# Optimization experiments

Hardware: AMD Instinct MI355X
Metric: run time of the kernel (lower is better)

Reference implementation:

```python
import jax, jax.numpy as jnp
import numpy as np

B, R, C, NC = 8, 1000, 1024, 81
H, W = 1024, 1024
MEANS = jnp.array([0.0, 0.0, 0.0, 0.0], jnp.float32)
STDS = jnp.array([0.1, 0.1, 0.2, 0.2], jnp.float32)
MIN_CONF = 0.05
NMS_THR = 0.5
MAX_INST = 100
NEG = -1e9


def setup_inputs() -> dict:
    key = jax.random.key(0)
    k1, k2, k3, k4, k5 = jax.random.split(key, 5)
    x = jax.random.normal(k1, (B * R, C), jnp.float32)
    w_cls = jax.random.normal(k2, (C, NC), jnp.float32) * 0.01
    b_cls = jnp.zeros((NC,), jnp.float32)
    w_delta = jax.random.normal(k3, (C, 4), jnp.float32) * 0.01
    b_delta = jnp.zeros((4,), jnp.float32)
    # rois: (batch_ind, y1, x1, y2, x2), normalized coords with y1<y2, x1<x2
    yx1 = jax.random.uniform(k4, (B * R, 2), jnp.float32) * 0.7
    hw = jax.random.uniform(k5, (B * R, 2), jnp.float32) * 0.28 + 0.02
    bind = jnp.repeat(jnp.arange(B, dtype=jnp.float32), R)[:, None]
    rois = jnp.concatenate([bind, yx1, yx1 + hw], axis=1)
    return {"x": x, "w_cls": w_cls, "b_cls": b_cls, "w_delta": w_delta, "b_delta": b_delta, "rois": rois}


def delta2bbox(rois, deltas):
    # rois, deltas: [N, 4] in (y1, x1, y2, x2) / (dy, dx, dh, dw)
    d = deltas * STDS + MEANS
    h = rois[:, 2] - rois[:, 0]
    w = rois[:, 3] - rois[:, 1]
    cy = rois[:, 0] + 0.5 * h + d[:, 0] * h
    cx = rois[:, 1] + 0.5 * w + d[:, 1] * w
    h = h * jnp.exp(d[:, 2])
    w = w * jnp.exp(d[:, 3])
    return jnp.stack([cy - 0.5 * h, cx - 0.5 * w, cy + 0.5 * h, cx + 0.5 * w], axis=1)


def pairwise_iou(boxes):
    # boxes: [N, 4]
    area = (boxes[:, 2] - boxes[:, 0]) * (boxes[:, 3] - boxes[:, 1])
    y1 = jnp.maximum(boxes[:, None, 0], boxes[None, :, 0])
    x1 = jnp.maximum(boxes[:, None, 1], boxes[None, :, 1])
    y2 = jnp.minimum(boxes[:, None, 2], boxes[None, :, 2])
    x2 = jnp.minimum(boxes[:, None, 3], boxes[None, :, 3])
    inter = jnp.maximum(y2 - y1, 0.0) * jnp.maximum(x2 - x1, 0.0)
    union = area[:, None] + area[None, :] - inter
    return inter / jnp.maximum(union, 1e-8)


def nms_single(boxes, scores, class_ids, valid):
    # boxes [R,4], scores [R], class_ids [R] int, valid [R] bool -> detections [MAX_INST, 6]
    masked = jnp.where(valid, scores, NEG)
    order = jnp.argsort(-masked)  # descending score
    b = boxes[order]
    s = masked[order]
    c = class_ids[order]
    v = valid[order]
    # class-aware IoU: cross-class pairs never suppress each other
    iou = pairwise_iou(b) * (c[:, None] == c[None, :]).astype(boxes.dtype)
    n = b.shape[0]

    def step(supp, xs):
        i, iou_row, vi = xs
        keep_i = vi & ~supp[i]
        supp = supp | jnp.where(keep_i, iou_row > NMS_THR, False)
        return supp, keep_i

    _, keep = jax.lax.scan(step, jnp.zeros((n,), bool), (jnp.arange(n), iou, v))
    final = jnp.where(keep, s, NEG)
    top_s, top_i = jax.lax.top_k(final, MAX_INST)
    ok = (top_s > NEG / 2)[:, None]
    det = jnp.concatenate([b[top_i], c[top_i].astype(boxes.dtype)[:, None], s[top_i][:, None]], axis=1)
    return jnp.where(ok, det, 0.0)


def reference(x, w_cls, b_cls, w_delta, b_delta, rois):
    logits = x @ w_cls + b_cls                      # [B*R, NC]
    probs = jax.nn.softmax(logits, axis=-1)
    deltas = x @ w_delta + b_delta                  # [B*R, 4]

    probs_b = probs.reshape(B, R, NC)
    class_ids = jnp.argmax(probs_b, axis=-1).astype(jnp.int32)           # [B, R]
    class_scores = jnp.take_along_axis(probs_b, class_ids[..., None], axis=-1)[..., 0]

    scale = jnp.array([H, W, H, W], jnp.float32)
    boxes = rois[:, 1:5] * scale                    # pixel coords, [B*R, 4]
    refined = delta2bbox(boxes, deltas)
    window = jnp.array([0.0, 0.0, float(H), float(W)], jnp.float32)
    refined = jnp.clip(refined, window[jnp.array([0, 1, 0, 1])], window[jnp.array([2, 3, 2, 3])])
    refined = refined.reshape(B, R, 4)

    valid = (class_ids > 0) & (class_scores >= MIN_CONF)
    detections = jax.vmap(nms_single)(refined, class_scores, class_ids, valid)  # [B, MAX_INST, 6]
    return detections
```

## Files before the change

### kernel.cpp

```cpp
#include <hip/hip_runtime.h>
#include <math.h>
#include <stdint.h>

#define RR 1000
#define CC 1024
#define NCLS 81
#define HH 1024.0f
#define MIN_CONF_V 0.05f
#define NMS_THR_V 0.5f
#define NEGV -1e9f

typedef __attribute__((ext_vector_type(8))) short bf16x8;
typedef __attribute__((ext_vector_type(4))) float f32x4;

__device__ __forceinline__ unsigned short f2bf(float f) {
    unsigned int u = __float_as_uint(f);
    return (unsigned short)((u + 0x7FFFu + ((u >> 16) & 1u)) >> 16);
}
__device__ __forceinline__ float bf2f(unsigned short h) {
    return __uint_as_float(((unsigned int)h) << 16);
}

__global__ __launch_bounds__(64) void k0_pack(
    const float* __restrict__ w_cls, const float* __restrict__ w_delta,
    unsigned short* __restrict__ wh, unsigned short* __restrict__ wl)
{
    const int ct = blockIdx.x >> 5;
    const int sg = blockIdx.x & 31;
    const int l = threadIdx.x;
    const int col = ct * 16 + (l & 15);
    const int kbase = sg * 32 + (l >> 4) * 8;
    unsigned short h[8], lo[8];
    #pragma unroll
    for (int j = 0; j < 8; ++j) {
        const int k = kbase + j;
        float v = 0.f;
        if (col < NCLS)          v = w_cls[(size_t)k * NCLS + col];
        else if (col < NCLS + 4) v = w_delta[(size_t)k * 4 + (col - NCLS)];
        h[j] = f2bf(v);
        lo[j] = f2bf(v - bf2f(h[j]));
    }
    const size_t base = ((size_t)(ct * 32 + sg) * 64 + l) * 8;
    uint4 uh, ul;
    uh.x = (unsigned)h[0] | ((unsigned)h[1] << 16);
    uh.y = (unsigned)h[2] | ((unsigned)h[3] << 16);
    uh.z = (unsigned)h[4] | ((unsigned)h[5] << 16);
    uh.w = (unsigned)h[6] | ((unsigned)h[7] << 16);
    ul.x = (unsigned)lo[0] | ((unsigned)lo[1] << 16);
    ul.y = (unsigned)lo[2] | ((unsigned)lo[3] << 16);
    ul.z = (unsigned)lo[4] | ((unsigned)lo[5] << 16);
    ul.w = (unsigned)lo[6] | ((unsigned)lo[7] << 16);
    *(uint4*)&wh[base] = uh;
    *(uint4*)&wl[base] = ul;
}

__global__ __launch_bounds__(384) void k1_head(
    const float* __restrict__ x,
    const unsigned short* __restrict__ wh, const unsigned short* __restrict__ wl,
    const float* __restrict__ b_cls, const float* __restrict__ b_delta,
    const float* __restrict__ rois,
    float* __restrict__ bx_ws, float* __restrict__ sc_ws, float* __restrict__ cid_ws)
{
    __shared__ __align__(16) unsigned short xh[2][32][64];
    __shared__ __align__(16) unsigned short xl[2][32][64];
    __shared__ float outb[32 * 104];

    const int t = threadIdx.x;
    const int lane = t & 63;
    const int ct = t >> 6;
    const int row0 = blockIdx.x * 32;

    const int srow0 = t >> 4;
    const int sc4 = t & 15;
    const int sd0 = (sc4 ^ ((srow0 & 7) << 1)) * 4;
    const size_t xsrc0 = (size_t)(row0 + srow0) * CC + sc4 * 4;
    const int srow1 = 24 + (t >> 4);
    const int sd1 = (sc4 ^ ((srow1 & 7) << 1)) * 4;
    const size_t xsrc1 = (size_t)(row0 + srow1) * CC + sc4 * 4;

    const int r = lane & 15;
    const int m = lane >> 4;
    const int e2 = (r & 7) << 1;
    const int a00 = r * 64        + (((m << 1) + 0) ^ e2) * 4;
    const int a01 = r * 64        + (((m << 1) + 8) ^ e2) * 4;
    const int a10 = (r + 16) * 64 + (((m << 1) + 0) ^ e2) * 4;
    const int a11 = (r + 16) * 64 + (((m << 1) + 8) ^ e2) * 4;

    const unsigned short* whp = wh + ((size_t)(ct * 32) * 64 + lane) * 8;
    const unsigned short* wlp = wl + ((size_t)(ct * 32) * 64 + lane) * 8;
    const size_t bstep = 64 * 8;

    f32x4 acc0 = {0.f, 0.f, 0.f, 0.f};
    f32x4 acc1 = {0.f, 0.f, 0.f, 0.f};

    float4 xv0 = *(const float4*)(x + xsrc0);
    float4 xv1 = make_float4(0.f, 0.f, 0.f, 0.f);
    if (t < 128) xv1 = *(const float4*)(x + xsrc1);

    bf16x8 B0h = *(const bf16x8*)(whp + 0 * bstep);
    bf16x8 B0l = *(const bf16x8*)(wlp + 0 * bstep);
    bf16x8 B1h = *(const bf16x8*)(whp + 1 * bstep);
    bf16x8 B1l = *(const bf16x8*)(wlp + 1 * bstep);

    int cur = 0;
    for (int c = 0; c < 16; ++c) {
        {
            unsigned short h0 = f2bf(xv0.x), h1 = f2bf(xv0.y), h2 = f2bf(xv0.z), h3 = f2bf(xv0.w);
            *(ushort4*)&xh[cur][srow0][sd0] = make_ushort4(h0, h1, h2, h3);
            *(ushort4*)&xl[cur][srow0][sd0] = make_ushort4(
                f2bf(xv0.x - bf2f(h0)), f2bf(xv0.y - bf2f(h1)),
                f2bf(xv0.z - bf2f(h2)), f2bf(xv0.w - bf2f(h3)));
            if (t < 128) {
                unsigned short g0 = f2bf(xv1.x), g1 = f2bf(xv1.y), g2 = f2bf(xv1.z), g3 = f2bf(xv1.w);
                *(ushort4*)&xh[cur][srow1][sd1] = make_ushort4(g0, g1, g2, g3);
                *(ushort4*)&xl[cur][srow1][sd1] = make_ushort4(
                    f2bf(xv1.x - bf2f(g0)), f2bf(xv1.y - bf2f(g1)),
                    f2bf(xv1.z - bf2f(g2)), f2bf(xv1.w - bf2f(g3)));
            }
        }
        __syncthreads();

        bf16x8 N0h = B0h, N0l = B0l, N1h = B1h, N1l = B1l;
        if (c < 15) {
            const size_t off = (size_t)(c + 1) * 64;
            xv0 = *(const float4*)(x + xsrc0 + off);
            if (t < 128) xv1 = *(const float4*)(x + xsrc1 + off);
            const size_t sg = (size_t)(2 * c + 2);
            N0h = *(const bf16x8*)(whp + sg * bstep);
            N0l = *(const bf16x8*)(wlp + sg * bstep);
            N1h = *(const bf16x8*)(whp + (sg + 1) * bstep);
            N1l = *(const bf16x8*)(wlp + (sg + 1) * bstep);
        }

        const unsigned short* hb = (const unsigned short*)xh[cur];
        const unsigned short* lb = (const unsigned short*)xl[cur];
        const bf16x8 a0h = *(const bf16x8*)(hb + a00);
        const bf16x8 a0l = *(const bf16x8*)(lb + a00);
        const bf16x8 a2h = *(const bf16x8*)(hb + a10);
        const bf16x8 a2l = *(const bf16x8*)(lb + a10);
        acc0 = __builtin_amdgcn_mfma_f32_16x16x32_bf16(a0h, B0h, acc0, 0, 0, 0);
        acc1 = __builtin_amdgcn_mfma_f32_16x16x32_bf16(a2h, B0h, acc1, 0, 0, 0);
        acc0 = __builtin_amdgcn_mfma_f32_16x16x32_bf16(a0h, B0l, acc0, 0, 0, 0);
        acc1 = __builtin_amdgcn_mfma_f32_16x16x32_bf16(a2h, B0l, acc1, 0, 0, 0);
        acc0 = __builtin_amdgcn_mfma_f32_16x16x32_bf16(a0l, B0h, acc0, 0, 0, 0);
        acc1 = __builtin_amdgcn_mfma_f32_16x16x32_bf16(a2l, B0h, acc1, 0, 0, 0);
        const bf16x8 a1h = *(const bf16x8*)(hb + a01);
        const bf16x8 a1l = *(const bf16x8*)(lb + a01);
        const bf16x8 a3h = *(const bf16x8*)(hb + a11);
        const bf16x8 a3l = *(const bf16x8*)(lb + a11);
        acc0 = __builtin_amdgcn_mfma_f32_16x16x32_bf16(a1h, B1h, acc0, 0, 0, 0);
        acc1 = __builtin_amdgcn_mfma_f32_16x16x32_bf16(a3h, B1h, acc1, 0, 0, 0);
        acc0 = __builtin_amdgcn_mfma_f32_16x16x32_bf16(a1h, B1l, acc0, 0, 0, 0);
        acc1 = __builtin_amdgcn_mfma_f32_16x16x32_bf16(a3h, B1l, acc1, 0, 0, 0);
        acc0 = __builtin_amdgcn_mfma_f32_16x16x32_bf16(a1l, B1h, acc0, 0, 0, 0);
        acc1 = __builtin_amdgcn_mfma_f32_16x16x32_bf16(a3l, B1h, acc1, 0, 0, 0);

        B0h = N0h; B0l = N0l; B1h = N1h; B1l = N1l;
        cur ^= 1;
        __syncthreads();
    }

    #pragma unroll
    for (int rr = 0; rr < 4; ++rr) {
        outb[((lane >> 4) * 4 + rr) * 104 + ct * 16 + (lane & 15)] = acc0[rr];
        outb[((lane >> 4) * 4 + rr + 16) * 104 + ct * 16 + (lane & 15)] = acc1[rr];
    }
    __syncthreads();

    if (t < 256) {
        const int row = t >> 3;
        const int e = t & 7;
        float vmax = -INFINITY;
        int imax = 1 << 20;
        float v[12];
        #pragma unroll
        for (int s = 0; s < 12; ++s) {
            const int cidx = e + 8 * s;
            if (cidx < NCLS) {
                const float val = outb[row * 104 + cidx] + b_cls[cidx];
                v[s] = val;
                if (val > vmax) { vmax = val; imax = cidx; }
            } else v[s] = -INFINITY;
        }
        #pragma unroll
        for (int mm = 4; mm >= 1; mm >>= 1) {
            const float v2 = __shfl_xor(vmax, mm);
            const int   i2 = __shfl_xor(imax, mm);
            if (v2 > vmax || (v2 == vmax && i2 < imax)) { vmax = v2; imax = i2; }
        }
        float sume = 0.f;
        #pragma unroll
        for (int s = 0; s < 12; ++s) {
            const int cidx = e + 8 * s;
            if (cidx < NCLS) sume += expf(v[s] - vmax);
        }
        #pragma unroll
        for (int mm = 4; mm >= 1; mm >>= 1) sume += __shfl_xor(sume, mm);

        if (e == 0) {
            const int gr = row0 + row;
            const float score = 1.0f / sume;
            const int cid = imax;
            const float d0 = (outb[row * 104 + 81] + b_delta[0]) * 0.1f;
            const float d1 = (outb[row * 104 + 82] + b_delta[1]) * 0.1f;
            const float d2 = (outb[row * 104 + 83] + b_delta[2]) * 0.2f;
            const float d3 = (outb[row * 104 + 84] + b_delta[3]) * 0.2f;
            const float y1 = rois[(size_t)gr * 5 + 1] * HH;
            const float x1 = rois[(size_t)gr * 5 + 2] * HH;
            const float y2 = rois[(size_t)gr * 5 + 3] * HH;
            const float x2 = rois[(size_t)gr * 5 + 4] * HH;
            const float h = y2 - y1, w = x2 - x1;
            const float cy = y1 + 0.5f * h + d0 * h;
            const float cx = x1 + 0.5f * w + d1 * w;
            const float h2 = h * expf(d2);
            const float w2 = w * expf(d3);
            const float by1 = fminf(fmaxf(cy - 0.5f * h2, 0.f), HH);
            const float bx1 = fminf(fmaxf(cx - 0.5f * w2, 0.f), HH);
            const float by2 = fminf(fmaxf(cy + 0.5f * h2, 0.f), HH);
            const float bx2 = fminf(fmaxf(cx + 0.5f * w2, 0.f), HH);
            const bool valid = (cid > 0) && (score >= MIN_CONF_V);
            bx_ws[(size_t)gr * 4 + 0] = by1;
            bx_ws[(size_t)gr * 4 + 1] = bx1;
            bx_ws[(size_t)gr * 4 + 2] = by2;
            bx_ws[(size_t)gr * 4 + 3] = bx2;
            sc_ws[gr]  = valid ? score : NEGV;
            cid_ws[gr] = (float)cid;
        }
    }
}

__global__ __launch_bounds__(256) void k2_nms(
    const float* __restrict__ bx_ws, const float* __restrict__ sc_ws,
    const float* __restrict__ cid_ws, float* __restrict__ det)
{
    __shared__ unsigned long long keys[256];
    __shared__ float sy1[256], sx1[256], sy2[256], sx2[256];
    __shared__ float scl[256], ssc[256];
    __shared__ unsigned char supp[256];
    __shared__ int s_cnt, s_num;

    const int b = blockIdx.x;
    const int t = threadIdx.x;
    const int base = b * RR;

    keys[t] = 0ull;
    if (t == 0) { s_cnt = 0; s_num = 0; }
    __syncthreads();

    for (int r = t; r < RR; r += 256) {
        const float s = sc_ws[base + r];
        if (s > NEGV * 0.5f) {
            const int i = atomicAdd(&s_num, 1);
            if (i < 256) {
                unsigned int u = __float_as_uint(s) | 0x80000000u;
                keys[i] = ((unsigned long long)u << 32) | (unsigned int)(~(unsigned int)r);
            }
        }
    }
    __syncthreads();
    const int V = (s_num < 256) ? s_num : 256;

    for (int k = 2; k <= 256; k <<= 1) {
        for (int j = k >> 1; j > 0; j >>= 1) {
            const int ixj = t ^ j;
            if (ixj > t) {
                const unsigned long long a = keys[t];
                const unsigned long long c = keys[ixj];
                const bool desc = ((t & k) == 0);
                if (desc ? (a < c) : (a > c)) { keys[t] = c; keys[ixj] = a; }
            }
            __syncthreads();
        }
    }

    if (t < V) {
        const int orig = (int)(~(unsigned int)keys[t]);
        const int g = base + orig;
        sy1[t] = bx_ws[(size_t)g * 4 + 0];
        sx1[t] = bx_ws[(size_t)g * 4 + 1];
        sy2[t] = bx_ws[(size_t)g * 4 + 2];
        sx2[t] = bx_ws[(size_t)g * 4 + 3];
        scl[t] = cid_ws[g];
        ssc[t] = sc_ws[g];
    } else {
        sy1[t] = sx1[t] = sy2[t] = sx2[t] = 0.f;
        scl[t] = -1.f;
        ssc[t] = NEGV;
    }
    supp[t] = 0;
    __syncthreads();

    for (int i = 0; i < V; ++i) {
        __syncthreads();
        if (s_cnt >= 100) break;
        if (!supp[i]) {
            if (t > i && t < V && scl[t] == scl[i]) {
                const float yy1 = fmaxf(sy1[i], sy1[t]);
                const float xx1 = fmaxf(sx1[i], sx1[t]);
                const float yy2 = fminf(sy2[i], sy2[t]);
                const float xx2 = fminf(sx2[i], sx2[t]);
                const float inter = fmaxf(yy2 - yy1, 0.f) * fmaxf(xx2 - xx1, 0.f);
                const float ai = (sy2[i] - sy1[i]) * (sx2[i] - sx1[i]);
                const float at = (sy2[t] - sy1[t]) * (sx2[t] - sx1[t]);
                const float uni = ai + at - inter;
                if (inter / fmaxf(uni, 1e-8f) > NMS_THR_V) supp[t] = 1;
            }
            if (t == 0) {
                const int slot = s_cnt;
                if (slot < 100) {
                    float* o = det + ((size_t)b * 100 + slot) * 6;
                    o[0] = sy1[i]; o[1] = sx1[i]; o[2] = sy2[i]; o[3] = sx2[i];
                    o[4] = scl[i]; o[5] = ssc[i];
                }
                s_cnt = slot + 1;
            }
        }
    }
    __syncthreads();
    int cnt = s_cnt;
    if (cnt > 100) cnt = 100;
    for (int idx = t; idx < 600; idx += 256) {
        if (idx >= cnt * 6) det[(size_t)b * 600 + idx] = 0.f;
    }
}

extern "C" void kernel_launch(void* const* d_in, const int* in_sizes, int n_in,
                              void* d_out, int out_size, void* d_ws, size_t ws_size,
                              hipStream_t stream) {
    const float* x       = (const float*)d_in[0];
    const float* w_cls   = (const float*)d_in[1];
    const float* b_cls   = (const float*)d_in[2];
    const float* w_delta = (const float*)d_in[3];
    const float* b_delta = (const float*)d_in[4];
    const float* rois    = (const float*)d_in[5];
    float* out = (float*)d_out;

    float* bx_ws   = (float*)d_ws;
    float* sc_ws   = bx_ws + 8000 * 4;
    float* cid_ws  = sc_ws + 8000;
    unsigned short* wh = (unsigned short*)(cid_ws + 8000);
    unsigned short* wl = wh + 98304;

    k0_pack<<<192, 64, 0, stream>>>(w_cls, w_delta, wh, wl);
    k1_head<<<250, 384, 0, stream>>>(x, wh, wl, b_cls, b_delta, rois,
                                     bx_ws, sc_ws, cid_ws);
    k2_nms<<<8, 256, 0, stream>>>(bx_ws, sc_ws, cid_ws, out);
}
```

Baseline: 33.14 us.

## Stage four K-chunks per barrier in head GEMM with deeper register prefetch

Restructures the k1_head main loop so each iteration converts four 64-wide K-chunks of x into shared memory (8 LDS buffers, double-buffered in groups of 4), cutting barriers from 32 to 8. Global loads for the next four chunks are issued before the MFMAs of the current group, which increases memory-level parallelism. In exchange it uses four times the LDS for x (about 64KB total) and more registers for prefetched x, which may lower occupancy. The NMS loop variable rename is cosmetic.

```diff
diff --git a/kernel.cpp b/kernel.cpp
--- a/kernel.cpp
+++ b/kernel.cpp
@@ -61,8 +61,8 @@
     const float* __restrict__ rois,
     float* __restrict__ bx_ws, float* __restrict__ sc_ws, float* __restrict__ cid_ws)
 {
-    __shared__ __align__(16) unsigned short xh[2][32][64];
-    __shared__ __align__(16) unsigned short xl[2][32][64];
+    __shared__ __align__(16) unsigned short xh[8][32][64];
+    __shared__ __align__(16) unsigned short xl[8][32][64];
     __shared__ float outb[32 * 104];
 
     const int t = threadIdx.x;
@@ -93,70 +93,92 @@
     f32x4 acc0 = {0.f, 0.f, 0.f, 0.f};
     f32x4 acc1 = {0.f, 0.f, 0.f, 0.f};
 
-    float4 xv0 = *(const float4*)(x + xsrc0);
-    float4 xv1 = make_float4(0.f, 0.f, 0.f, 0.f);
-    if (t < 128) xv1 = *(const float4*)(x + xsrc1);
+    float4 xr0[4];
+    float4 xr1[4];
+    #pragma unroll
+    for (int c = 0; c < 4; ++c) {
+        xr0[c] = *(const float4*)(x + xsrc0 + (size_t)c * 64);
+        if (t < 128) xr1[c] = *(const float4*)(x + xsrc1 + (size_t)c * 64);
+    }
 
     bf16x8 B0h = *(const bf16x8*)(whp + 0 * bstep);
     bf16x8 B0l = *(const bf16x8*)(wlp + 0 * bstep);
     bf16x8 B1h = *(const bf16x8*)(whp + 1 * bstep);
     bf16x8 B1l = *(const bf16x8*)(wlp + 1 * bstep);
 
-    int cur = 0;
-    for (int c = 0; c < 16; ++c) {
-        {
-            unsigned short h0 = f2bf(xv0.x), h1 = f2bf(xv0.y), h2 = f2bf(xv0.z), h3 = f2bf(xv0.w);
-            *(ushort4*)&xh[cur][srow0][sd0] = make_ushort4(h0, h1, h2, h3);
-            *(ushort4*)&xl[cur][srow0][sd0] = make_ushort4(
-                f2bf(xv0.x - bf2f(h0)), f2bf(xv0.y - bf2f(h1)),
-                f2bf(xv0.z - bf2f(h2)), f2bf(xv0.w - bf2f(h3)));
+    for (int sc = 0; sc < 4; ++sc) {
+        #pragma unroll
+        for (int c = 0; c < 4; ++c) {
+            const int buf = (sc & 1) * 4 + c;
+            {
+                const float4 v = xr0[c];
+                const unsigned short h0 = f2bf(v.x), h1 = f2bf(v.y),
+                                     h2 = f2bf(v.z), h3 = f2bf(v.w);
+                *(ushort4*)&xh[buf][srow0][sd0] = make_ushort4(h0, h1, h2, h3);
+                *(ushort4*)&xl[buf][srow0][sd0] = make_ushort4(
+                    f2bf(v.x - bf2f(h0)), f2bf(v.y - bf2f(h1)),
+                    f2bf(v.z - bf2f(h2)), f2bf(v.w - bf2f(h3)));
+            }
             if (t < 128) {
-                unsigned short g0 = f2bf(xv1.x), g1 = f2bf(xv1.y), g2 = f2bf(xv1.z), g3 = f2bf(xv1.w);
-                *(ushort4*)&xh[cur][srow1][sd1] = make_ushort4(g0, g1, g2, g3);
-                *(ushort4*)&xl[cur][srow1][sd1] = make_ushort4(
-                    f2bf(xv1.x - bf2f(g0)), f2bf(xv1.y - bf2f(g1)),
-                    f2bf(xv1.z - bf2f(g2)), f2bf(xv1.w - bf2f(g3)));
+                const float4 v = xr1[c];
+                const unsigned short g0 = f2bf(v.x), g1 = f2bf(v.y),
+                                     g2 = f2bf(v.z), g3 = f2bf(v.w);
+                *(ushort4*)&xh[buf][srow1][sd1] = make_ushort4(g0, g1, g2, g3);
+                *(ushort4*)&xl[buf][srow1][sd1] = make_ushort4(
+                    f2bf(v.x - bf2f(g0)), f2bf(v.y - bf2f(g1)),
+                    f2bf(v.z - bf2f(g2)), f2bf(v.w - bf2f(g3)));
             }
         }
         __syncthreads();
 
-        bf16x8 N0h = B0h, N0l = B0l, N1h = B1h, N1l = B1l;
-        if (c < 15) {
-            const size_t off = (size_t)(c + 1) * 64;
-            xv0 = *(const float4*)(x + xsrc0 + off);
-            if (t < 128) xv1 = *(const float4*)(x + xsrc1 + off);
-            const size_t sg = (size_t)(2 * c + 2);
-            N0h = *(const bf16x8*)(whp + sg * bstep);
-            N0l = *(const bf16x8*)(wlp + sg * bstep);
-            N1h = *(const bf16x8*)(whp + (sg + 1) * bstep);
-            N1l = *(const bf16x8*)(wlp + (sg + 1) * bstep);
-        }
-
-        const unsigned short* hb = (const unsigned short*)xh[cur];
-        const unsigned short* lb = (const unsigned short*)xl[cur];
-        const bf16x8 a0h = *(const bf16x8*)(hb + a00);
-        const bf16x8 a0l = *(const bf16x8*)(lb + a00);
-        const bf16x8 a2h = *(const bf16x8*)(hb + a10);
-        const bf16x8 a2l = *(const bf16x8*)(lb + a10);
-        acc0 = __builtin_amdgcn_mfma_f32_16x16x32_bf16(a0h, B0h, acc0, 0, 0, 0);
-        acc1 = __builtin_amdgcn_mfma_f32_16x16x32_bf16(a2h, B0h, acc1, 0, 0, 0);
-        acc0 = __builtin_amdgcn_mfma_f32_16x16x32_bf16(a0h, B0l, acc0, 0, 0, 0);
-        acc1 = __builtin_amdgcn_mfma_f32_16x16x32_bf16(a2h, B0l, acc1, 0, 0, 0);
-        acc0 = __builtin_amdgcn_mfma_f32_16x16x32_bf16(a0l, B0h, acc0, 0, 0, 0);
-        acc1 = __builtin_amdgcn_mfma_f32_16x16x32_bf16(a2l, B0h, acc1, 0, 0, 0);
-        const bf16x8 a1h = *(const bf16x8*)(hb + a01);
-        const bf16x8 a1l = *(const bf16x8*)(lb + a01);
-        const bf16x8 a3h = *(const bf16x8*)(hb + a11);
-        const bf16x8 a3l = *(const bf16x8*)(lb + a11);
-        acc0 = __builtin_amdgcn_mfma_f32_16x16x32_bf16(a1h, B1h, acc0, 0, 0, 0);
-        acc1 = __builtin_amdgcn_mfma_f32_16x16x32_bf16(a3h, B1h, acc1, 0, 0, 0);
-        acc0 = __builtin_amdgcn_mfma_f32_16x16x32_bf16(a1h, B1l, acc0, 0, 0, 0);
-        acc1 = __builtin_amdgcn_mfma_f32_16x16x32_bf16(a3h, B1l, acc1, 0, 0, 0);
-        acc0 = __builtin_amdgcn_mfma_f32_16x16x32_bf16(a1l, B1h, acc0, 0, 0, 0);
-        acc1 = __builtin_amdgcn_mfma_f32_16x16x32_bf16(a3l, B1h, acc1, 0, 0, 0);
-
-        B0h = N0h; B0l = N0l; B1h = N1h; B1l = N1l;
-        cur ^= 1;
+        if (sc < 3) {
+            #pragma unroll
+            for (int c = 0; c < 4; ++c) {
+                const size_t off = (size_t)((sc + 1) * 4 + c) * 64;
+                xr0[c] = *(const float4*)(x + xsrc0 + off);
+                if (t < 128) xr1[c] = *(const float4*)(x + xsrc1 + off);
+            }
+        }
+
+        #pragma unroll
+        for (int c = 0; c < 4; ++c) {
+            const int ch = sc * 4 + c;
+            const int buf = (sc & 1) * 4 + c;
+
+            bf16x8 N0h = B0h, N0l = B0l, N1h = B1h, N1l = B1l;
+            if (ch < 15) {
+                const size_t sg = (size_t)(2 * ch + 2);
+                N0h = *(const bf16x8*)(whp + sg * bstep);
+                N0l = *(const bf16x8*)(wlp + sg * bstep);
+                N1h = *(const bf16x8*)(whp + (sg + 1) * bstep);
+                N1l = *(const bf16x8*)(wlp + (sg + 1) * bstep);
+            }
+
+            const unsigned short* hb = (const unsigned short*)xh[buf];
+            const unsigned short* lb = (const unsigned short*)xl[buf];
+            const bf16x8 a0h = *(const bf16x8*)(hb + a00);
+            const bf16x8 a0l = *(const bf16x8*)(lb + a00);
+            const bf16x8 a2h = *(const bf16x8*)(hb + a10);
+            const bf16x8 a2l = *(const bf16x8*)(lb + a10);
+            acc0 = __builtin_amdgcn_mfma_f32_16x16x32_bf16(a0h, B0h, acc0, 0, 0, 0);
+            acc1 = __builtin_amdgcn_mfma_f32_16x16x32_bf16(a2h, B0h, acc1, 0, 0, 0);
+            acc0 = __builtin_amdgcn_mfma_f32_16x16x32_bf16(a0h, B0l, acc0, 0, 0, 0);
+            acc1 = __builtin_amdgcn_mfma_f32_16x16x32_bf16(a2h, B0l, acc1, 0, 0, 0);
+            acc0 = __builtin_amdgcn_mfma_f32_16x16x32_bf16(a0l, B0h, acc0, 0, 0, 0);
+            acc1 = __builtin_amdgcn_mfma_f32_16x16x32_bf16(a2l, B0h, acc1, 0, 0, 0);
+            const bf16x8 a1h = *(const bf16x8*)(hb + a01);
+            const bf16x8 a1l = *(const bf16x8*)(lb + a01);
+            const bf16x8 a3h = *(const bf16x8*)(hb + a11);
+            const bf16x8 a3l = *(const bf16x8*)(lb + a11);
+            acc0 = __builtin_amdgcn_mfma_f32_16x16x32_bf16(a1h, B1h, acc0, 0, 0, 0);
+            acc1 = __builtin_amdgcn_mfma_f32_16x16x32_bf16(a3h, B1h, acc1, 0, 0, 0);
+            acc0 = __builtin_amdgcn_mfma_f32_16x16x32_bf16(a1h, B1l, acc0, 0, 0, 0);
+            acc1 = __builtin_amdgcn_mfma_f32_16x16x32_bf16(a3h, B1l, acc1, 0, 0, 0);
+            acc0 = __builtin_amdgcn_mfma_f32_16x16x32_bf16(a1l, B1h, acc0, 0, 0, 0);
+            acc1 = __builtin_amdgcn_mfma_f32_16x16x32_bf16(a3l, B1h, acc1, 0, 0, 0);
+
+            B0h = N0h; B0l = N0l; B1h = N1h; B1l = N1l;
+        }
         __syncthreads();
     }
 
@@ -247,13 +269,13 @@
     if (t == 0) { s_cnt = 0; s_num = 0; }
     __syncthreads();
 
-    for (int r = t; r < RR; r += 256) {
-        const float s = sc_ws[base + r];
+    for (int rr = t; rr < RR; rr += 256) {
+        const float s = sc_ws[base + rr];
         if (s > NEGV * 0.5f) {
             const int i = atomicAdd(&s_num, 1);
             if (i < 256) {
                 unsigned int u = __float_as_uint(s) | 0x80000000u;
-                keys[i] = ((unsigned long long)u << 32) | (unsigned int)(~(unsigned int)r);
+                keys[i] = ((unsigned long long)u << 32) | (unsigned int)(~(unsigned int)rr);
             }
         }
     }
```

New measurement: 33.76 us. Within noise of the previous version (+1.9%).
